# Optimization experiments

Hardware: AMD Instinct MI355X
Metric: run time of the kernel (lower is better)

Reference implementation:

```python
import jax, jax.numpy as jnp
import numpy as np

N = 524288          # batch == input_size (original code feeds the (N,) ndi vector straight into Linear(input_size,10))
K = 66              # knots: torch.linspace(0, 1, 66)
_xk = np.linspace(0.0, 1.0, K).astype(np.float32)
_dx = np.diff(_xk).astype(np.float32)  # (K-1,), uniform h = 1/65


def _notaknot_matrix():
    # scipy.interpolate.CubicSpline default bc_type='not-a-knot': solve A @ s = b for the
    # first derivatives s at the knots. Interior rows are the standard tridiagonal C2 conditions;
    # first/last rows enforce continuity of the third derivative (not-a-knot).
    A = np.zeros((K, K), np.float32)
    dx = _dx
    i = np.arange(1, K - 1)
    A[i, i - 1] = dx[1:]
    A[i, i] = 2.0 * (dx[1:] + dx[:-1])
    A[i, i + 1] = dx[:-1]
    A[0, 0] = dx[1]
    A[0, 1] = _xk[2] - _xk[0]
    A[-1, -1] = dx[-2]
    A[-1, -2] = _xk[-1] - _xk[-3]
    return A

_A = _notaknot_matrix()


def _fit(y):
    # y: (N, K). Returns per-interval secant slopes (N, K-1) and knot derivatives s (N, K).
    dx = jnp.asarray(_dx)
    slope = (y[:, 1:] - y[:, :-1]) / dx
    d02 = float(_xk[2] - _xk[0])
    dl = float(_xk[-1] - _xk[-3])
    dx0 = float(_dx[0]); dx1 = float(_dx[1]); dxm1 = float(_dx[-1]); dxm2 = float(_dx[-2])
    b0 = ((dx0 + 2.0 * d02) * dx1 * slope[:, 0] + dx0 * dx0 * slope[:, 1]) / d02
    bl = (dxm1 * dxm1 * slope[:, -2] + (2.0 * dl + dxm1) * dxm2 * slope[:, -1]) / dl
    bi = 3.0 * (dx[1:] * slope[:, :-1] + dx[:-1] * slope[:, 1:])  # (N, K-2)
    b = jnp.concatenate([b0[:, None], bi, bl[:, None]], axis=1)   # (N, K)
    s = jnp.linalg.solve(jnp.asarray(_A), b.T).T                  # factor A once, N RHS
    return slope, s


def _eval(y, slope, s, t):
    # Evaluate every row's spline at scalar t (Hermite form, matches scipy coefficients).
    xk = jnp.asarray(_xk)
    k = jnp.clip(jnp.searchsorted(xk, t, side='right') - 1, 0, K - 2)
    h = xk[k + 1] - xk[k]
    u = t - xk[k]
    sk = s[:, k]
    sk1 = s[:, k + 1]
    mk = slope[:, k]
    tt = (sk + sk1 - 2.0 * mk) / h
    c0 = tt / h
    c1 = (mk - sk) / h - tt
    return ((c0 * u + c1) * u + sk) * u + y[:, k]


def setup_inputs() -> dict:
    key = jax.random.key(0)
    ks = jax.random.split(key, 6)
    x = jax.random.uniform(ks[0], (N, K), jnp.float32)
    soc = jax.random.uniform(ks[1], (N,), jnp.float32)
    lim1 = float(1.0 / np.sqrt(N))
    W1 = jax.random.uniform(ks[2], (10, N), jnp.float32, -lim1, lim1)
    b1 = jax.random.uniform(ks[3], (10,), jnp.float32, -lim1, lim1)
    lim2 = float(1.0 / np.sqrt(10.0))
    W2 = jax.random.uniform(ks[4], (1, 10), jnp.float32, -lim2, lim2)
    b2 = jax.random.uniform(ks[5], (1,), jnp.float32, -lim2, lim2)
    return {"x": x, "soc": soc, "i": jnp.asarray(0.1, jnp.float32), "j": jnp.asarray(0.9, jnp.float32),
            "W1": W1, "b1": b1, "W2": W2, "b2": b2}


def reference(x, soc, i, j, W1, b1, W2, b2):
    slope, s = _fit(x)
    r_i = _eval(x, slope, s, i)   # (N,)
    r_j = _eval(x, slope, s, j)   # (N,)
    ndis = (r_i - r_j) / (r_i + r_j)           # (N,)
    h1 = W1 @ ndis + b1                        # (10,)  -- original feeds 1-D ndis into Linear
    h1 = jnp.where(h1 > 0, h1, 0.01 * h1)      # LeakyReLU(0.01)
    soc_hat = W2 @ h1 + b2                     # (1,)
    loss = jnp.sum((soc_hat - soc) ** 2)       # MSELoss(reduction='sum') with broadcasting
    return soc_hat, ndis, loss
```

## Files before the change

### kernel.cpp

```cpp
#include <hip/hip_runtime.h>

#define NROW 524288
#define KDIM 66
#define NSEG 65
#define NB   2048
#define TILES (NROW / 64)
#define PART_STRIDE 12

#define WOFF_P 528

struct Pre {
    float  xk[KDIM];
    float  dxf[NSEG];
    double av[KDIM];
    double winv[KDIM];
    double cp[KDIM];
    double dxinv[NSEG];
    double d3[NSEG];
    double pp, qq, r1, r2;
};

constexpr Pre make_pre() {
    Pre p{};
    for (int k = 0; k < KDIM; ++k) p.xk[k] = (float)((1.0 / 65.0) * (double)k);
    p.xk[KDIM - 1] = 1.0f;
    for (int k = 0; k < NSEG; ++k) p.dxf[k] = p.xk[k + 1] - p.xk[k];

    double d02 = (double)(p.xk[2] - p.xk[0]);
    double dl  = (double)(p.xk[KDIM - 1] - p.xk[KDIM - 3]);

    double bv[KDIM] = {};
    double cv[KDIM] = {};
    bv[0] = (double)p.dxf[1];
    bv[KDIM - 1] = (double)p.dxf[KDIM - 3];
    for (int i = 1; i < KDIM - 1; ++i)
        bv[i] = 2.0 * ((double)p.dxf[i] + (double)p.dxf[i - 1]);
    p.av[0] = 0.0;
    p.av[1] = d02;
    for (int i = 2; i < KDIM; ++i) p.av[i] = (double)p.dxf[i - 2];
    for (int i = 0; i < KDIM - 2; ++i) cv[i] = (double)p.dxf[i + 1];
    cv[KDIM - 2] = dl;
    cv[KDIM - 1] = 0.0;

    double w = bv[0];
    p.winv[0] = 1.0 / w;
    p.cp[0]   = cv[0] / w;
    for (int i = 1; i < KDIM; ++i) {
        w = bv[i] - p.av[i] * p.cp[i - 1];
        p.winv[i] = 1.0 / w;
        p.cp[i]   = cv[i] / w;
    }
    for (int m = 0; m < NSEG; ++m) {
        p.dxinv[m] = 1.0 / (double)p.dxf[m];
        p.d3[m]    = 3.0 * (double)p.dxf[m];
    }
    p.pp = ((double)p.dxf[0] + 2.0 * d02) * (double)p.dxf[1] / d02;
    p.qq = (double)p.dxf[0] * (double)p.dxf[0] / d02;
    p.r1 = (double)p.dxf[64] * (double)p.dxf[64] / dl;
    p.r2 = (2.0 * dl + (double)p.dxf[64]) * (double)p.dxf[63] / dl;
    return p;
}

__device__ constexpr Pre PRE = make_pre();

__global__ __launch_bounds__(64) void setup_kernel(const float* __restrict__ ti,
                                                   const float* __restrict__ tj,
                                                   float* __restrict__ wout) {
    __shared__ double dp_s[2][KDIM];
    __shared__ double z_s[2][KDIM];
    const int tid = threadIdx.x;
    if (tid >= 2) return;
    const float t = (tid == 0) ? ti[0] : tj[0];
    float* wo = wout + tid * KDIM;

    int kk = 0;
    float xkk = PRE.xk[0], xkk1 = PRE.xk[1];
#pragma unroll
    for (int k = 0; k <= KDIM - 2; ++k) {
        if (PRE.xk[k] <= t) { kk = k; xkk = PRE.xk[k]; xkk1 = PRE.xk[k + 1]; }
    }

    const double h  = (double)(xkk1 - xkk);
    const double u  = (double)(t - xkk);
    const double u2 = u * u, u3 = u2 * u, h2 = h * h;
    const double alpha = u3 / h2 - 2.0 * u2 / h + u;
    const double beta  = u3 / h2 - u2 / h;
    const double gamma = 3.0 * u2 / h - 2.0 * u3 / h2;

    double dpv = 0.0;
#pragma unroll
    for (int i = 0; i < KDIM; ++i) {
        double rhs = (i == kk) ? alpha : ((i == kk + 1) ? beta : 0.0);
        dpv = (rhs - PRE.av[i] * dpv) * PRE.winv[i];
        dp_s[tid][i] = dpv;
    }

    double zv = dp_s[tid][KDIM - 1];
    z_s[tid][KDIM - 1] = zv;
#pragma unroll
    for (int i = KDIM - 2; i >= 0; --i) {
        zv = dp_s[tid][i] - PRE.cp[i] * zv;
        z_s[tid][i] = zv;
    }

    const double z0  = z_s[tid][0];
    const double z65 = z_s[tid][KDIM - 1];
    double c = z0 * PRE.pp;
    double carryW = 0.0;
#pragma unroll
    for (int j = 1; j <= 64; ++j) {
        const double zj = z_s[tid][j];
        double full = c + zj * PRE.d3[j];
        if (j - 1 == kk) full += gamma;
        if (j == 64)     full += z65 * PRE.r1;
        const double w = full * PRE.dxinv[j - 1];
        double wy = carryW - w;
        if (j - 1 == kk) wy += 1.0;
        wo[j - 1] = (float)wy;
        carryW = w;
        c = zj * PRE.d3[j - 1];
        if (j == 1) c += z0 * PRE.qq;
    }
    double full64 = c + z65 * PRE.r2;
    if (kk == 64) full64 += gamma;
    const double w64 = full64 * PRE.dxinv[64];
    double wy64 = carryW - w64;
    if (kk == 64) wy64 += 1.0;
    wo[64] = (float)wy64;
    wo[65] = (float)w64;
}

__global__ __launch_bounds__(64) void main_kernel(
    const float* __restrict__ x, const float* __restrict__ soc,
    const float* __restrict__ W1, const float* __restrict__ wglob,
    float* __restrict__ out_ndis, double* __restrict__ partials)
{
    __shared__ float tile[64 * KDIM];
    __shared__ float wlds[2 * KDIM];
    const int lane = threadIdx.x;

    wlds[lane]      = wglob[lane];
    wlds[64 + lane] = wglob[64 + lane];
    if (lane < 2 * KDIM - 128) wlds[128 + lane] = wglob[128 + lane];

    double accw[10];
#pragma unroll
    for (int o = 0; o < 10; ++o) accw[o] = 0.0;
    double accs = 0.0, accs2 = 0.0;

    for (int t = blockIdx.x; t < TILES; t += NB) {
        const int n = t * 64 + lane;

        float w1v[10];
#pragma unroll
        for (int o = 0; o < 10; ++o) w1v[o] = W1[(size_t)o * NROW + n];
        float socv = soc[n];

        __syncthreads();
        const float4* __restrict__ src4 =
            (const float4*)(x + (size_t)t * (64 * KDIM));
        float4* dst4 = (float4*)tile;
#pragma unroll
        for (int it = 0; it < 16; ++it)
            dst4[it * 64 + lane] = src4[it * 64 + lane];
        const float2* __restrict__ src2 =
            (const float2*)(x + (size_t)t * (64 * KDIM)) + 2048;
        ((float2*)tile)[2048 + lane] = src2[lane];
        __syncthreads();

        const float2* row = (const float2*)tile + lane * (KDIM / 2);
        const float2* wi2 = (const float2*)wlds;
        const float2* wj2 = wi2 + (KDIM / 2);
        float ri = 0.f, rj = 0.f;
#pragma unroll
        for (int k = 0; k < KDIM / 2; ++k) {
            float2 v = row[k];
            float2 a = wi2[k];
            float2 b = wj2[k];
            ri = fmaf(v.x, a.x, ri); ri = fmaf(v.y, a.y, ri);
            rj = fmaf(v.x, b.x, rj); rj = fmaf(v.y, b.y, rj);
        }

        float nd = (ri - rj) / (ri + rj);
        out_ndis[n] = nd;

        double ndd = (double)nd;
#pragma unroll
        for (int o = 0; o < 10; ++o)
            accw[o] = fma((double)w1v[o], ndd, accw[o]);
        double sv = (double)socv;
        accs  += sv;
        accs2  = fma(sv, sv, accs2);
    }

#pragma unroll
    for (int o = 0; o < 10; ++o) {
        double v = accw[o];
#pragma unroll
        for (int off = 32; off > 0; off >>= 1) v += __shfl_down(v, off, 64);
        accw[o] = v;
    }
    {
        double v = accs;
#pragma unroll
        for (int off = 32; off > 0; off >>= 1) v += __shfl_down(v, off, 64);
        accs = v;
        v = accs2;
#pragma unroll
        for (int off = 32; off > 0; off >>= 1) v += __shfl_down(v, off, 64);
        accs2 = v;
    }
    if (lane == 0) {
        double* p = partials + (size_t)blockIdx.x * PART_STRIDE;
#pragma unroll
        for (int o = 0; o < 10; ++o) p[o] = accw[o];
        p[10] = accs;
        p[11] = accs2;
    }
}

__global__ void finalize_kernel(const double* __restrict__ partials,
                                const float* __restrict__ b1,
                                const float* __restrict__ W2,
                                const float* __restrict__ b2,
                                float* __restrict__ out)
{
    __shared__ double red[16][16];
    __shared__ double totals[12];
    int tid = threadIdx.x;
    int o = tid & 15, g = tid >> 4;
    double s = 0.0;
    if (o < 12) {
        for (int b = g; b < NB; b += 16)
            s += partials[(size_t)b * PART_STRIDE + o];
    }
    red[g][o] = s;
    __syncthreads();
    if (tid < 12) {
        double tot = 0.0;
        for (int g2 = 0; g2 < 16; ++g2) tot += red[g2][tid];
        totals[tid] = tot;
    }
    __syncthreads();
    if (tid == 0) {
        double acc = 0.0;
#pragma unroll
        for (int o2 = 0; o2 < 10; ++o2) {
            double h1 = totals[o2] + (double)b1[o2];
            h1 = (h1 > 0.0) ? h1 : 0.01 * h1;
            acc += (double)W2[o2] * h1;
        }
        double shat = acc + (double)b2[0];
        out[0] = (float)shat;
        double ssum = totals[10], ssum2 = totals[11];
        double loss = (double)NROW * shat * shat - 2.0 * shat * ssum + ssum2;
        out[1 + NROW] = (float)loss;
    }
}

extern "C" void kernel_launch(void* const* d_in, const int* in_sizes, int n_in,
                              void* d_out, int out_size, void* d_ws, size_t ws_size,
                              hipStream_t stream) {
    const float* x   = (const float*)d_in[0];
    const float* soc = (const float*)d_in[1];
    const float* ti  = (const float*)d_in[2];
    const float* tj  = (const float*)d_in[3];
    const float* W1  = (const float*)d_in[4];
    const float* b1  = (const float*)d_in[5];
    const float* W2  = (const float*)d_in[6];
    const float* b2  = (const float*)d_in[7];
    float* out = (float*)d_out;

    float*  wglob    = (float*)d_ws;
    double* partials = (double*)((char*)d_ws + WOFF_P);

    setup_kernel<<<1, 64, 0, stream>>>(ti, tj, wglob);
    main_kernel<<<NB, 64, 0, stream>>>(x, soc, W1, wglob, out + 1, partials);
    finalize_kernel<<<1, 256, 0, stream>>>(partials, b1, W2, b2, out);
}
```

Baseline: 279.1 us.

## Map one row per thread with 256-thread blocks and direct global row loads

Replaces the 64-thread, grid-stride loop that staged 64-row tiles through LDS with 256-thread blocks where each thread reads its own row of x straight from global memory. The aim is more waves in flight to hide memory latency and no per-tile barriers or LDS staging. Each block now merges its four per-wave results through a small shared array before writing partials. The cost is that per-thread row reads are strided by 264 bytes across a wavefront, so loads are poorly coalesced and depend on cache reuse.

After: 278.7 us. Within noise of the previous version (-0.1%).

```diff
diff --git a/kernel.cpp b/kernel.cpp
--- a/kernel.cpp
+++ b/kernel.cpp
@@ -4,7 +4,6 @@
 #define KDIM 66
 #define NSEG 65
 #define NB   2048
-#define TILES (NROW / 64)
 #define PART_STRIDE 12
 
 #define WOFF_P 528
@@ -130,92 +129,68 @@
     wo[65] = (float)w64;
 }
 
-__global__ __launch_bounds__(64) void main_kernel(
+__global__ __launch_bounds__(256) void main_kernel(
     const float* __restrict__ x, const float* __restrict__ soc,
     const float* __restrict__ W1, const float* __restrict__ wglob,
     float* __restrict__ out_ndis, double* __restrict__ partials)
 {
-    __shared__ float tile[64 * KDIM];
-    __shared__ float wlds[2 * KDIM];
-    const int lane = threadIdx.x;
-
-    wlds[lane]      = wglob[lane];
-    wlds[64 + lane] = wglob[64 + lane];
-    if (lane < 2 * KDIM - 128) wlds[128 + lane] = wglob[128 + lane];
-
-    double accw[10];
-#pragma unroll
-    for (int o = 0; o < 10; ++o) accw[o] = 0.0;
-    double accs = 0.0, accs2 = 0.0;
-
-    for (int t = blockIdx.x; t < TILES; t += NB) {
-        const int n = t * 64 + lane;
-
-        float w1v[10];
-#pragma unroll
-        for (int o = 0; o < 10; ++o) w1v[o] = W1[(size_t)o * NROW + n];
-        float socv = soc[n];
-
-        __syncthreads();
-        const float4* __restrict__ src4 =
-            (const float4*)(x + (size_t)t * (64 * KDIM));
-        float4* dst4 = (float4*)tile;
-#pragma unroll
-        for (int it = 0; it < 16; ++it)
-            dst4[it * 64 + lane] = src4[it * 64 + lane];
-        const float2* __restrict__ src2 =
-            (const float2*)(x + (size_t)t * (64 * KDIM)) + 2048;
-        ((float2*)tile)[2048 + lane] = src2[lane];
-        __syncthreads();
-
-        const float2* row = (const float2*)tile + lane * (KDIM / 2);
-        const float2* wi2 = (const float2*)wlds;
-        const float2* wj2 = wi2 + (KDIM / 2);
-        float ri = 0.f, rj = 0.f;
-#pragma unroll
-        for (int k = 0; k < KDIM / 2; ++k) {
-            float2 v = row[k];
-            float2 a = wi2[k];
-            float2 b = wj2[k];
-            ri = fmaf(v.x, a.x, ri); ri = fmaf(v.y, a.y, ri);
-            rj = fmaf(v.x, b.x, rj); rj = fmaf(v.y, b.y, rj);
-        }
-
-        float nd = (ri - rj) / (ri + rj);
-        out_ndis[n] = nd;
-
-        double ndd = (double)nd;
-#pragma unroll
-        for (int o = 0; o < 10; ++o)
-            accw[o] = fma((double)w1v[o], ndd, accw[o]);
-        double sv = (double)socv;
-        accs  += sv;
-        accs2  = fma(sv, sv, accs2);
-    }
-
-#pragma unroll
-    for (int o = 0; o < 10; ++o) {
-        double v = accw[o];
+    __shared__ __align__(16) float wi_s[KDIM];
+    __shared__ __align__(16) float wj_s[KDIM];
+    __shared__ double red[4][12];
+    const int tid = threadIdx.x;
+
+    if (tid < KDIM)            wi_s[tid]        = wglob[tid];
+    else if (tid < 2 * KDIM)   wj_s[tid - KDIM] = wglob[tid];
+    __syncthreads();
+
+    const int n = blockIdx.x * 256 + tid;
+
+    float w1v[10];
+#pragma unroll
+    for (int o = 0; o < 10; ++o) w1v[o] = W1[(size_t)o * NROW + n];
+    const float socv = soc[n];
+
+    const float2* __restrict__ row = (const float2*)(x + (size_t)n * KDIM);
+    const float2* wi2 = (const float2*)wi_s;
+    const float2* wj2 = (const float2*)wj_s;
+    float ri = 0.f, rj = 0.f;
+#pragma unroll
+    for (int k = 0; k < KDIM / 2; ++k) {
+        const float2 v = row[k];
+        const float2 a = wi2[k];
+        const float2 b = wj2[k];
+        ri = fmaf(v.x, a.x, ri); ri = fmaf(v.y, a.y, ri);
+        rj = fmaf(v.x, b.x, rj); rj = fmaf(v.y, b.y, rj);
+    }
+
+    const float nd = (ri - rj) / (ri + rj);
+    out_ndis[n] = nd;
+
+    const double ndd = (double)nd;
+    double acc[12];
+#pragma unroll
+    for (int o = 0; o < 10; ++o) acc[o] = (double)w1v[o] * ndd;
+    const double sv = (double)socv;
+    acc[10] = sv;
+    acc[11] = sv * sv;
+
+#pragma unroll
+    for (int o = 0; o < 12; ++o) {
+        double v = acc[o];
 #pragma unroll
         for (int off = 32; off > 0; off >>= 1) v += __shfl_down(v, off, 64);
-        accw[o] = v;
-    }
-    {
-        double v = accs;
-#pragma unroll
-        for (int off = 32; off > 0; off >>= 1) v += __shfl_down(v, off, 64);
-        accs = v;
-        v = accs2;
-#pragma unroll
-        for (int off = 32; off > 0; off >>= 1) v += __shfl_down(v, off, 64);
-        accs2 = v;
-    }
+        acc[o] = v;
+    }
+    const int wid  = tid >> 6;
+    const int lane = tid & 63;
     if (lane == 0) {
-        double* p = partials + (size_t)blockIdx.x * PART_STRIDE;
-#pragma unroll
-        for (int o = 0; o < 10; ++o) p[o] = accw[o];
-        p[10] = accs;
-        p[11] = accs2;
+#pragma unroll
+        for (int o = 0; o < 12; ++o) red[wid][o] = acc[o];
+    }
+    __syncthreads();
+    if (tid < 12) {
+        double s = red[0][tid] + red[1][tid] + red[2][tid] + red[3][tid];
+        partials[(size_t)blockIdx.x * PART_STRIDE + tid] = s;
     }
 }
 
@@ -275,6 +250,6 @@
     double* partials = (double*)((char*)d_ws + WOFF_P);
 
     setup_kernel<<<1, 64, 0, stream>>>(ti, tj, wglob);
-    main_kernel<<<NB, 64, 0, stream>>>(x, soc, W1, wglob, out + 1, partials);
+    main_kernel<<<NB, 256, 0, stream>>>(x, soc, W1, wglob, out + 1, partials);
     finalize_kernel<<<1, 256, 0, stream>>>(partials, b1, W2, b2, out);
 }
```
